# Kernel tuning notes

Measured on AMD Instinct MI355X. Metric: run time of the kernel, lower is better.

The kernel has to match this reference:

```python
import jax, jax.numpy as jnp
import numpy as np

ROUTE_NUM = 3
EPS = 1e-8


def squash(s):
    # s: [bs, J, d2]; squash along last dim
    sq = jnp.sum(s * s, axis=-1, keepdims=True)
    return (sq / (1.0 + sq)) * s / jnp.sqrt(sq + EPS)


def setup_inputs() -> dict:
    key = jax.random.key(0)
    k1, k2, k3 = jax.random.split(key, 3)
    bs, in_dim, s1 = 64, 256, 16
    out_dim, J = 32, 64           # J = num_out_caps (as_final_output)
    I = s1 * s1                   # num_in_caps = 256
    x = jax.random.normal(k1, (bs, in_dim, s1, s1), dtype=jnp.float32)
    b_init = jax.random.uniform(k2, (bs, J, I), dtype=jnp.float32)
    W = jax.random.normal(k3, (out_dim * J, in_dim), dtype=jnp.float32) * 0.05
    Wb = jnp.zeros((out_dim * J,), dtype=jnp.float32)
    return {"x": x, "b_init": b_init, "W": W, "Wb": Wb}


def reference(x, b_init, W, Wb):
    bs = x.shape[0]
    J, I = b_init.shape[1], b_init.shape[2]
    d2 = W.shape[0] // J
    # 1x1 conv == per-pixel GEMM: [bs, OUT, s1, s1]
    pred = jnp.einsum('oi,bihw->bohw', W, x) + Wb[None, :, None, None]
    # [bs, J, d2, I] -> [bs, I, J, d2]
    pred = pred.reshape(bs, J, d2, I).transpose(0, 3, 1, 2)
    b = b_init
    v = None
    for _ in range(ROUTE_NUM):
        c = jax.nn.softmax(b, axis=1)                  # softmax over out-caps J
        s = jnp.einsum('bji,bijd->bjd', c, pred)       # weighted sum over in-caps
        v = squash(s)                                  # [bs, J, d2]
        db = jax.lax.stop_gradient(jnp.einsum('bjd,bijd->bji', v, pred))
        b = b + db
    return v
```

## Files before the change

### kernel.cpp

```cpp
#include <hip/hip_runtime.h>
#include <hip/hip_bf16.h>

#define BS    64
#define KDIM  256
#define ICAP  256
#define JCAP  64
#define D2    32
#define OUTD  2048
#define NPART 16

typedef short bf16x8 __attribute__((ext_vector_type(8)));
typedef float f32x4  __attribute__((ext_vector_type(4)));

static __device__ __forceinline__ float bf2f(unsigned u16) {
  union { unsigned u; float f; } v; v.u = u16 << 16; return v.f;
}
static __device__ __forceinline__ unsigned short f2bf(float x) {
  union { float f; unsigned u; } v; v.f = x;
  unsigned r = v.u + 0x7fffu + ((v.u >> 16) & 1u);
  return (unsigned short)(r >> 16);
}
static __device__ __forceinline__ void unpack8(uint4 u, float* f) {
  f[0] = bf2f(u.x & 0xffffu); f[1] = bf2f(u.x >> 16);
  f[2] = bf2f(u.y & 0xffffu); f[3] = bf2f(u.y >> 16);
  f[4] = bf2f(u.z & 0xffffu); f[5] = bf2f(u.z >> 16);
  f[6] = bf2f(u.w & 0xffffu); f[7] = bf2f(u.w >> 16);
}
static __device__ __forceinline__ void gl_lds16(const unsigned short* g,
                                                unsigned short* l) {
  __builtin_amdgcn_global_load_lds(
      (const __attribute__((address_space(1))) unsigned int*)g,
      (__attribute__((address_space(3))) unsigned int*)l, 16, 0, 0);
}

__global__ __launch_bounds__(256) void prep(
    const float* __restrict__ W, const float* __restrict__ x,
    const float* __restrict__ Binit,
    unsigned short* __restrict__ Wbf, unsigned short* __restrict__ xT,
    unsigned short* __restrict__ c0)
{
  __shared__ union {
    float Ls[64][65];
    float Bs[64][68];
  } sm;
  const int t   = threadIdx.x;
  const int blk = blockIdx.x;

  if (blk < 256) {
    const int g = blk * 256 + t;
    const float* s = W + (size_t)g * 8;
    f32x4 a = *(const f32x4*)s;
    f32x4 b = *(const f32x4*)(s + 4);
    uint4 o;
    o.x = (unsigned)f2bf(a.x) | ((unsigned)f2bf(a.y) << 16);
    o.y = (unsigned)f2bf(a.z) | ((unsigned)f2bf(a.w) << 16);
    o.z = (unsigned)f2bf(b.x) | ((unsigned)f2bf(b.y) << 16);
    o.w = (unsigned)f2bf(b.z) | ((unsigned)f2bf(b.w) << 16);
    *(uint4*)(Wbf + (size_t)g * 8) = o;
  } else if (blk < 1280) {
    const int bid = blk - 256;
    const int i0  = (bid & 3) * 64;
    const int k0  = ((bid >> 2) & 3) * 64;
    const int b   = bid >> 4;
    for (int it = 0; it < 4; ++it) {
      const int k  = it * 16 + (t >> 4);
      const int i4 = (t & 15) * 4;
      f32x4 v = *(const f32x4*)(x + ((size_t)(b * KDIM + k0 + k) * ICAP) + i0 + i4);
      sm.Ls[k][i4 + 0] = v.x; sm.Ls[k][i4 + 1] = v.y;
      sm.Ls[k][i4 + 2] = v.z; sm.Ls[k][i4 + 3] = v.w;
    }
    __syncthreads();
    const int i  = t >> 2;
    const int kc = (t & 3) * 16;
    unsigned pk[8];
    for (int q = 0; q < 8; ++q) {
      float lo = sm.Ls[kc + 2 * q][i];
      float hi = sm.Ls[kc + 2 * q + 1][i];
      pk[q] = (unsigned)f2bf(lo) | ((unsigned)f2bf(hi) << 16);
    }
    unsigned short* dst = xT + ((size_t)(b * ICAP + i0 + i) * KDIM) + k0 + kc;
    uint4 s0; s0.x = pk[0]; s0.y = pk[1]; s0.z = pk[2]; s0.w = pk[3];
    uint4 s1; s1.x = pk[4]; s1.y = pk[5]; s1.z = pk[6]; s1.w = pk[7];
    *(uint4*)dst       = s0;
    *(uint4*)(dst + 8) = s1;
  } else {
    const int bid = blk - 1280;
    const int b   = bid >> 2;
    const int q   = bid & 3;
    {
      const int j  = t >> 2;
      const int c4 = (t & 3) * 16;
      const float* src = Binit + ((size_t)(b * JCAP + j) * ICAP) + q * 64 + c4;
      for (int r = 0; r < 4; ++r) {
        f32x4 v = *(const f32x4*)(src + r * 4);
        *(f32x4*)&sm.Bs[j][c4 + r * 4] = v;
      }
    }
    __syncthreads();
    if (t < 64) {
      const int ii = t;
      float m = -3.0e38f;
      for (int j = 0; j < 64; ++j) m = fmaxf(m, sm.Bs[j][ii]);
      float se = 0.f;
      for (int j = 0; j < 64; ++j) se += __expf(sm.Bs[j][ii] - m);
      const float inv = 1.0f / se;
      unsigned short* dst = c0 + ((size_t)(b * ICAP + q * 64 + ii) * JCAP);
      for (int qq = 0; qq < 8; ++qq) {
        unsigned pk[4];
        for (int h = 0; h < 4; ++h) {
          float lo = __expf(sm.Bs[qq * 8 + 2 * h][ii] - m) * inv;
          float hi = __expf(sm.Bs[qq * 8 + 2 * h + 1][ii] - m) * inv;
          pk[h] = (unsigned)f2bf(lo) | ((unsigned)f2bf(hi) << 16);
        }
        uint4 s; s.x = pk[0]; s.y = pk[1]; s.z = pk[2]; s.w = pk[3];
        *(uint4*)(dst + qq * 8) = s;
      }
    }
  }
}

__global__ __launch_bounds__(256) void gemm_pred(
    const unsigned short* __restrict__ Wbf,
    const unsigned short* __restrict__ xT,
    const float* __restrict__ Wb,
    const unsigned short* __restrict__ c0,
    unsigned short* __restrict__ P,
    float* __restrict__ s0part)
{
  __shared__ union {
    unsigned short AB[2][128][64];
    struct {
      unsigned short C[64][136];
      unsigned short c0t[128][4];
    } ep;
  } sm;

  const int tid = threadIdx.x;
  const int b   = blockIdx.z;
  const int o0  = blockIdx.x * 128;
  const int i0  = blockIdx.y * 128;
  const int l   = tid & 63;
  const int m   = l & 15;
  const int w   = tid >> 6;
  const int wo  = (w & 1) * 64;

  const int srow = l >> 3;
  const int gch  = (l & 7) ^ srow;

  f32x4 acc[4][4];
  for (int a = 0; a < 4; ++a)
    for (int c = 0; c < 4; ++c) acc[a][c] = (f32x4){0.f, 0.f, 0.f, 0.f};

  for (int r = 0; r < 4; ++r) {
    const int k0 = r * 64;
    __syncthreads();
    for (int c = 0; c < 4; ++c) {
      const int q   = w * 4 + c;
      const int row = q * 8 + srow;
      gl_lds16(Wbf + (size_t)(o0 + row) * KDIM + k0 + gch * 8,
               &sm.AB[0][q * 8][0]);
      gl_lds16(xT + ((size_t)(b * ICAP + i0 + row) * KDIM) + k0 + gch * 8,
               &sm.AB[1][q * 8][0]);
    }
    __syncthreads();
    for (int ks = 0; ks < 2; ++ks) {
      const int clog = ks * 4 + (l >> 4);
      bf16x8 af[4], bfg[4];
      for (int ti = 0; ti < 4; ++ti) {
        const int row = wo + 16 * ti + m;
        af[ti] = *(const bf16x8*)&sm.AB[0][row][(clog ^ (m & 7)) * 8];
      }
      for (int tj = 0; tj < 4; ++tj) {
        const int row = (w >> 1) * 64 + 16 * tj + m;
        bfg[tj] = *(const bf16x8*)&sm.AB[1][row][(clog ^ (m & 7)) * 8];
      }
      for (int ti = 0; ti < 4; ++ti)
        for (int tj = 0; tj < 4; ++tj)
          acc[ti][tj] = __builtin_amdgcn_mfma_f32_16x16x32_bf16(
              af[ti], bfg[tj], acc[ti][tj], 0, 0, 0);
    }
  }

  __syncthreads();
  if (tid < 128) {
    const int j0 = blockIdx.x * 4;
    uint2 v = *(const uint2*)(c0 + ((size_t)(b * ICAP + i0 + tid) * JCAP) + j0);
    *(uint2*)&sm.ep.c0t[tid][0] = v;
  }

  for (int half = 0; half < 2; ++half) {
    __syncthreads();
    if ((w >> 1) == half) {
      const int q4 = (l >> 4) * 4;
      for (int ti = 0; ti < 4; ++ti) {
        const int ob = wo + 16 * ti + q4;
        f32x4 wb4 = *(const f32x4*)(Wb + o0 + ob);
        for (int tj = 0; tj < 4; ++tj) {
          const int ii = 16 * tj + m;
          f32x4 a = acc[ti][tj];
          uint2 pk;
          pk.x = (unsigned)f2bf(a.x + wb4.x) | ((unsigned)f2bf(a.y + wb4.y) << 16);
          pk.y = (unsigned)f2bf(a.z + wb4.z) | ((unsigned)f2bf(a.w + wb4.w) << 16);
          *(uint2*)&sm.ep.C[ii][ob] = pk;
        }
      }
    }
    __syncthreads();
    for (int rr = 0; rr < 4; ++rr) {
      const int id  = rr * 256 + tid;
      const int row = id >> 4;
      const int seg = id & 15;
      uint4 v = *(const uint4*)&sm.ep.C[row][seg * 8];
      *(uint4*)(P + ((size_t)(b * ICAP + i0 + half * 64 + row) * OUTD) + o0 + seg * 8) = v;
    }
    {
      const int oc = tid & 127;
      const int q  = tid >> 7;
      const int jj = oc >> 5;
      float s = 0.f;
      for (int r2 = 0; r2 < 32; ++r2) {
        const int il = q * 32 + r2;
        s += bf2f(sm.ep.C[il][oc]) * bf2f(sm.ep.c0t[half * 64 + il][jj]);
      }
      const int p = blockIdx.y * 4 + half * 2 + q;
      s0part[((size_t)(b * 8 + p) * OUTD) + o0 + oc] = s;
    }
  }
}

__global__ __launch_bounds__(256) void squash_v(
    const float* __restrict__ part,
    const int npart,
    float* __restrict__ dst)
{
  const int tid = threadIdx.x;
  const int b   = blockIdx.x;
  const float* base = part + (size_t)b * npart * OUTD + tid * 8;
  float s[8] = {0.f,0.f,0.f,0.f,0.f,0.f,0.f,0.f};
  for (int p = 0; p < npart; ++p) {
    f32x4 a = *(const f32x4*)(base + (size_t)p * OUTD);
    f32x4 c = *(const f32x4*)(base + (size_t)p * OUTD + 4);
    s[0] += a.x; s[1] += a.y; s[2] += a.z; s[3] += a.w;
    s[4] += c.x; s[5] += c.y; s[6] += c.z; s[7] += c.w;
  }
  float sq = 0.f;
  for (int c = 0; c < 8; ++c) sq += s[c] * s[c];
  sq += __shfl_xor(sq, 1, 64);
  sq += __shfl_xor(sq, 2, 64);
  float scale = (sq / (1.0f + sq)) / sqrtf(sq + 1e-8f);
  float* d = dst + (size_t)b * OUTD + tid * 8;
  f32x4 t0 = {scale*s[0], scale*s[1], scale*s[2], scale*s[3]};
  f32x4 t1 = {scale*s[4], scale*s[5], scale*s[6], scale*s[7]};
  *(f32x4*)d       = t0;
  *(f32x4*)(d + 4) = t1;
}

__global__ __launch_bounds__(256) void route_fused(
    const unsigned short* __restrict__ P,
    const float* __restrict__ Binit,
    const float* __restrict__ part_in,
    const int npart_in,
    const float* __restrict__ Vprev,
    float* __restrict__ Vout,
    float* __restrict__ part_out)
{
  __shared__ union {
    float Vs[2112];
    float Ps[4][2112];
  } sm;

  const int tid = threadIdx.x;
  const int l   = tid & 63;
  const int w   = tid >> 6;
  const int b   = blockIdx.x >> 4;
  const int g   = blockIdx.x & 15;

  {
    const float* base = part_in + (size_t)b * npart_in * OUTD + tid * 8;
    float s[8] = {0.f,0.f,0.f,0.f,0.f,0.f,0.f,0.f};
    for (int p = 0; p < npart_in; ++p) {
      f32x4 a = *(const f32x4*)(base + (size_t)p * OUTD);
      f32x4 c = *(const f32x4*)(base + (size_t)p * OUTD + 4);
      s[0] += a.x; s[1] += a.y; s[2] += a.z; s[3] += a.w;
      s[4] += c.x; s[5] += c.y; s[6] += c.z; s[7] += c.w;
    }
    float sq = 0.f;
    for (int c = 0; c < 8; ++c) sq += s[c] * s[c];
    sq += __shfl_xor(sq, 1, 64);
    sq += __shfl_xor(sq, 2, 64);
    float scale = (sq / (1.0f + sq)) / sqrtf(sq + 1e-8f);
    const int j  = tid >> 2;
    const int d0 = (tid & 3) * 8;
    float vloc[8];
    for (int c = 0; c < 8; ++c) vloc[c] = scale * s[c];
    if (Vout && g == 0) {
      float* vd = Vout + (size_t)b * OUTD + tid * 8;
      f32x4 t0 = {vloc[0], vloc[1], vloc[2], vloc[3]};
      f32x4 t1 = {vloc[4], vloc[5], vloc[6], vloc[7]};
      *(f32x4*)vd       = t0;
      *(f32x4*)(vd + 4) = t1;
    }
    if (Vprev) {
      const float* vp = Vprev + (size_t)b * OUTD + tid * 8;
      f32x4 t0 = *(const f32x4*)vp;
      f32x4 t1 = *(const f32x4*)(vp + 4);
      vloc[0] += t0.x; vloc[1] += t0.y; vloc[2] += t0.z; vloc[3] += t0.w;
      vloc[4] += t1.x; vloc[5] += t1.y; vloc[6] += t1.z; vloc[7] += t1.w;
    }
    for (int c = 0; c < 8; ++c) sm.Vs[j * 33 + d0 + c] = vloc[c];
  }
  __syncthreads();
  float vv[32];
  for (int k = 0; k < 32; ++k) vv[k] = sm.Vs[l * 33 + k];

  const int i0 = g * 16 + w * 4;
  float bold[4];
  {
    f32x4 t = *(const f32x4*)(Binit + (size_t)(b * JCAP + l) * ICAP + i0);
    bold[0] = t.x; bold[1] = t.y; bold[2] = t.z; bold[3] = t.w;
  }

  float sacc[32];
  for (int k = 0; k < 32; ++k) sacc[k] = 0.f;

  const unsigned short* pbase = P + ((size_t)(b * ICAP + i0) * OUTD) + l * D2;
  uint4 ubuf[2][4];
  for (int q = 0; q < 4; ++q) ubuf[0][q] = *(const uint4*)(pbase + q * 8);
  for (int q = 0; q < 4; ++q) ubuf[1][q] = *(const uint4*)(pbase + OUTD + q * 8);

#pragma unroll
  for (int ii = 0; ii < 4; ++ii) {
    uint4 cur[4];
    for (int q = 0; q < 4; ++q) cur[q] = ubuf[ii & 1][q];
    if (ii + 2 < 4)
      for (int q = 0; q < 4; ++q)
        ubuf[ii & 1][q] = *(const uint4*)(pbase + (size_t)(ii + 2) * OUTD + q * 8);

    float db = 0.f;
    for (int q = 0; q < 4; ++q) {
      float ps[8]; unpack8(cur[q], ps);
      for (int k = 0; k < 8; ++k) db += ps[k] * vv[q * 8 + k];
    }
    float bnew = bold[ii] + db;

    float mx = bnew;
    for (int off = 1; off < 64; off <<= 1) mx = fmaxf(mx, __shfl_xor(mx, off, 64));
    float e = __expf(bnew - mx);
    float se = e;
    for (int off = 1; off < 64; off <<= 1) se += __shfl_xor(se, off, 64);
    float c = e / se;
    for (int q = 0; q < 4; ++q) {
      float ps[8]; unpack8(cur[q], ps);
      for (int k = 0; k < 8; ++k) sacc[q * 8 + k] += c * ps[k];
    }
  }

  __syncthreads();
  for (int k = 0; k < 32; ++k) sm.Ps[w][l * 33 + k] = sacc[k];
  __syncthreads();

  {
    const int o0 = tid * 8;
    float s[8];
    for (int c = 0; c < 8; ++c) {
      const int o = o0 + c, j = o >> 5, d = o & 31, idx = j * 33 + d;
      s[c] = sm.Ps[0][idx] + sm.Ps[1][idx] + sm.Ps[2][idx] + sm.Ps[3][idx];
    }
    float* dst = part_out + ((size_t)(b * NPART + g)) * OUTD + o0;
    f32x4 t0 = {s[0], s[1], s[2], s[3]};
    f32x4 t1 = {s[4], s[5], s[6], s[7]};
    *(f32x4*)dst       = t0;
    *(f32x4*)(dst + 4) = t1;
  }
}

extern "C" void kernel_launch(void* const* d_in, const int* in_sizes, int n_in,
                              void* d_out, int out_size, void* d_ws, size_t ws_size,
                              hipStream_t stream) {
  const float* x  = (const float*)d_in[0];
  const float* bi = (const float*)d_in[1];
  const float* W  = (const float*)d_in[2];
  const float* Wb = (const float*)d_in[3];
  float* out = (float*)d_out;

  char* ws = (char*)d_ws;
  const size_t MiB = 1024 * 1024;
  unsigned short* P        = (unsigned short*)ws;
  unsigned short* xT       = (unsigned short*)(ws + 64 * MiB);
  float*          partial1 = (float*)(ws + 64 * MiB);
  float*          s0part   = (float*)(ws + 72 * MiB);
  unsigned short* Wbf      = (unsigned short*)(ws + 76 * MiB);
  unsigned short* c0       = (unsigned short*)(ws + 77 * MiB);
  float*          partial2 = (float*)(ws + 72 * MiB);
  float* V1                = (float*)(ws + 80 * MiB);

  prep<<<dim3(1536), 256, 0, stream>>>(W, x, bi, Wbf, xT, c0);
  gemm_pred<<<dim3(16, 2, 64), 256, 0, stream>>>(Wbf, xT, Wb, c0, P, s0part);
  route_fused<<<dim3(1024), 256, 0, stream>>>(P, bi, s0part, 8, nullptr, V1, partial1);
  route_fused<<<dim3(1024), 256, 0, stream>>>(P, bi, partial1, NPART, V1, nullptr, partial2);
  squash_v<<<dim3(64), 256, 0, stream>>>(partial2, NPART, out);
}
```

Baseline: 164.8 us.

## Compute GEMM epilogue from registers with shuffle reduction instead of LDS staging

The gemm_pred epilogue no longer stages the bf16 output tile through shared memory. Each lane now writes its 4-wide P fragments straight to global memory and accumulates the c0-weighted s0 partial sums in registers. A 16-lane xor-shuffle reduction then halves the number of s0 partitions from 8 to 4. This removes several barriers and the LDS round trip, and it lets the c0 load overlap with the main loop. The cost is narrower, less coalesced 8-byte global stores of P, and s0 is now summed from unrounded fp32 values rather than the bf16-rounded ones.

```diff
diff --git a/kernel.cpp b/kernel.cpp
--- a/kernel.cpp
+++ b/kernel.cpp
@@ -127,13 +127,8 @@
     unsigned short* __restrict__ P,
     float* __restrict__ s0part)
 {
-  __shared__ union {
-    unsigned short AB[2][128][64];
-    struct {
-      unsigned short C[64][136];
-      unsigned short c0t[128][4];
-    } ep;
-  } sm;
+  __shared__ unsigned short AB[2][128][64];
+  __shared__ unsigned short c0t[128][4];
 
   const int tid = threadIdx.x;
   const int b   = blockIdx.z;
@@ -141,8 +136,16 @@
   const int i0  = blockIdx.y * 128;
   const int l   = tid & 63;
   const int m   = l & 15;
+  const int q   = l >> 4;
   const int w   = tid >> 6;
   const int wo  = (w & 1) * 64;
+  const int wi  = (w >> 1) * 64;
+
+  if (tid < 128) {
+    const int j0 = blockIdx.x * 4;
+    uint2 v = *(const uint2*)(c0 + ((size_t)(b * ICAP + i0 + tid) * JCAP) + j0);
+    *(uint2*)&c0t[tid][0] = v;
+  }
 
   const int srow = l >> 3;
   const int gch  = (l & 7) ^ srow;
@@ -155,24 +158,24 @@
     const int k0 = r * 64;
     __syncthreads();
     for (int c = 0; c < 4; ++c) {
-      const int q   = w * 4 + c;
-      const int row = q * 8 + srow;
+      const int qq  = w * 4 + c;
+      const int row = qq * 8 + srow;
       gl_lds16(Wbf + (size_t)(o0 + row) * KDIM + k0 + gch * 8,
-               &sm.AB[0][q * 8][0]);
+               &AB[0][qq * 8][0]);
       gl_lds16(xT + ((size_t)(b * ICAP + i0 + row) * KDIM) + k0 + gch * 8,
-               &sm.AB[1][q * 8][0]);
+               &AB[1][qq * 8][0]);
     }
     __syncthreads();
     for (int ks = 0; ks < 2; ++ks) {
-      const int clog = ks * 4 + (l >> 4);
+      const int clog = ks * 4 + q;
       bf16x8 af[4], bfg[4];
       for (int ti = 0; ti < 4; ++ti) {
         const int row = wo + 16 * ti + m;
-        af[ti] = *(const bf16x8*)&sm.AB[0][row][(clog ^ (m & 7)) * 8];
+        af[ti] = *(const bf16x8*)&AB[0][row][(clog ^ (m & 7)) * 8];
       }
       for (int tj = 0; tj < 4; ++tj) {
-        const int row = (w >> 1) * 64 + 16 * tj + m;
-        bfg[tj] = *(const bf16x8*)&sm.AB[1][row][(clog ^ (m & 7)) * 8];
+        const int row = wi + 16 * tj + m;
+        bfg[tj] = *(const bf16x8*)&AB[1][row][(clog ^ (m & 7)) * 8];
       }
       for (int ti = 0; ti < 4; ++ti)
         for (int tj = 0; tj < 4; ++tj)
@@ -181,50 +184,39 @@
     }
   }
 
-  __syncthreads();
-  if (tid < 128) {
-    const int j0 = blockIdx.x * 4;
-    uint2 v = *(const uint2*)(c0 + ((size_t)(b * ICAP + i0 + tid) * JCAP) + j0);
-    *(uint2*)&sm.ep.c0t[tid][0] = v;
-  }
-
-  for (int half = 0; half < 2; ++half) {
-    __syncthreads();
-    if ((w >> 1) == half) {
-      const int q4 = (l >> 4) * 4;
-      for (int ti = 0; ti < 4; ++ti) {
-        const int ob = wo + 16 * ti + q4;
-        f32x4 wb4 = *(const f32x4*)(Wb + o0 + ob);
-        for (int tj = 0; tj < 4; ++tj) {
-          const int ii = 16 * tj + m;
-          f32x4 a = acc[ti][tj];
-          uint2 pk;
-          pk.x = (unsigned)f2bf(a.x + wb4.x) | ((unsigned)f2bf(a.y + wb4.y) << 16);
-          pk.y = (unsigned)f2bf(a.z + wb4.z) | ((unsigned)f2bf(a.w + wb4.w) << 16);
-          *(uint2*)&sm.ep.C[ii][ob] = pk;
-        }
-      }
-    }
-    __syncthreads();
-    for (int rr = 0; rr < 4; ++rr) {
-      const int id  = rr * 256 + tid;
-      const int row = id >> 4;
-      const int seg = id & 15;
-      uint4 v = *(const uint4*)&sm.ep.C[row][seg * 8];
-      *(uint4*)(P + ((size_t)(b * ICAP + i0 + half * 64 + row) * OUTD) + o0 + seg * 8) = v;
-    }
-    {
-      const int oc = tid & 127;
-      const int q  = tid >> 7;
-      const int jj = oc >> 5;
-      float s = 0.f;
-      for (int r2 = 0; r2 < 32; ++r2) {
-        const int il = q * 32 + r2;
-        s += bf2f(sm.ep.C[il][oc]) * bf2f(sm.ep.c0t[half * 64 + il][jj]);
-      }
-      const int p = blockIdx.y * 4 + half * 2 + q;
-      s0part[((size_t)(b * 8 + p) * OUTD) + o0 + oc] = s;
-    }
+  f32x4 s0q[4];
+  for (int ti = 0; ti < 4; ++ti) s0q[ti] = (f32x4){0.f, 0.f, 0.f, 0.f};
+
+  for (int ti = 0; ti < 4; ++ti) {
+    const int ob = wo + 16 * ti + 4 * q;
+    f32x4 wb4 = *(const f32x4*)(Wb + o0 + ob);
+    const int jloc = (wo >> 5) + (ti >> 1);
+    for (int tj = 0; tj < 4; ++tj) {
+      const int iloc = wi + 16 * tj + m;
+      f32x4 a = acc[ti][tj];
+      a.x += wb4.x; a.y += wb4.y; a.z += wb4.z; a.w += wb4.w;
+      uint2 pk;
+      pk.x = (unsigned)f2bf(a.x) | ((unsigned)f2bf(a.y) << 16);
+      pk.y = (unsigned)f2bf(a.z) | ((unsigned)f2bf(a.w) << 16);
+      *(uint2*)(P + ((size_t)(b * ICAP + i0 + iloc)) * OUTD + o0 + ob) = pk;
+      const float c0v = bf2f(c0t[iloc][jloc]);
+      s0q[ti].x += c0v * a.x; s0q[ti].y += c0v * a.y;
+      s0q[ti].z += c0v * a.z; s0q[ti].w += c0v * a.w;
+    }
+  }
+  for (int off = 1; off < 16; off <<= 1) {
+    for (int ti = 0; ti < 4; ++ti) {
+      s0q[ti].x += __shfl_xor(s0q[ti].x, off, 64);
+      s0q[ti].y += __shfl_xor(s0q[ti].y, off, 64);
+      s0q[ti].z += __shfl_xor(s0q[ti].z, off, 64);
+      s0q[ti].w += __shfl_xor(s0q[ti].w, off, 64);
+    }
+  }
+  if (m == 0) {
+    const int p = blockIdx.y * 2 + (wi >> 6);
+    float* dst = s0part + ((size_t)(b * 4 + p)) * OUTD + o0;
+    for (int ti = 0; ti < 4; ++ti)
+      *(f32x4*)(dst + wo + 16 * ti + 4 * q) = s0q[ti];
   }
 }
 
@@ -396,7 +388,7 @@
 
   prep<<<dim3(1536), 256, 0, stream>>>(W, x, bi, Wbf, xT, c0);
   gemm_pred<<<dim3(16, 2, 64), 256, 0, stream>>>(Wbf, xT, Wb, c0, P, s0part);
-  route_fused<<<dim3(1024), 256, 0, stream>>>(P, bi, s0part, 8, nullptr, V1, partial1);
+  route_fused<<<dim3(1024), 256, 0, stream>>>(P, bi, s0part, 4, nullptr, V1, partial1);
   route_fused<<<dim3(1024), 256, 0, stream>>>(P, bi, partial1, NPART, V1, nullptr, partial2);
   squash_v<<<dim3(64), 256, 0, stream>>>(partial2, NPART, out);
 }
```

Measured after the change: 164.8 us. Within noise of the previous version (-0.0%).
